# Kernel optimization log

Measured on AMD Instinct MI355X. Metric: run time of the kernel, lower is better.

The kernel has to match this reference:

```python
import jax, jax.numpy as jnp
import numpy as np

LOWERSIZE = 40


def setup_inputs() -> dict:
    key = jax.random.key(0)
    ks = jax.random.split(key, 6)
    N, x_dim, y_dim = 2048, 768, 768
    return {
        "x_samples": jax.random.normal(ks[0], (N, x_dim), dtype=jnp.float32),
        "y_samples": jax.random.normal(ks[1], (N, y_dim), dtype=jnp.float32),
        "W1": jax.random.normal(ks[2], (LOWERSIZE, x_dim + y_dim), dtype=jnp.float32) * 0.02,
        "b1": jax.random.normal(ks[3], (LOWERSIZE,), dtype=jnp.float32) * 0.02,
        "W2": jax.random.normal(ks[4], (1, LOWERSIZE), dtype=jnp.float32) * 0.02,
        "b2": jax.random.normal(ks[5], (1,), dtype=jnp.float32) * 0.02,
    }


def reference(x_samples, y_samples, W1, b1, W2, b2):
    # F(z) = W2 @ relu(W1 @ z + b1) + b2, z = cat(x, y)
    N = y_samples.shape[0]
    x_dim = x_samples.shape[1]
    W1x = W1[:, :x_dim]   # [40, x_dim]
    W1y = W1[:, x_dim:]   # [40, y_dim]

    # Diagonal term T0: F(cat(x_i, y_i)) -> [N, 1]
    h0 = jax.nn.relu(x_samples @ W1x.T + y_samples @ W1y.T + b1)
    T0 = h0 @ W2.T + b2

    # Pairwise term: T1[i, j] = F(cat(x_j, y_i)) - 1.
    # Split the first Linear over x and y to avoid materializing the
    # [N, N, x_dim+y_dim] concatenation (same math, linearity of W1).
    hx = x_samples @ W1x.T  # [N, 40]
    hy = y_samples @ W1y.T  # [N, 40]
    h = jax.nn.relu(hy[:, None, :] + hx[None, :, :] + b1)  # [N, N, 40]
    T1 = (h @ W2.T + b2 - 1.0)[..., 0]  # [N, N]

    lse = jax.nn.logsumexp(T1, axis=1) - jnp.log(jnp.float32(N))  # [N]
    lower_bound = T0.mean() - jnp.exp(lse).mean()
    return lower_bound
```

## Files before the change

kernel.cpp:

```cpp
#include <hip/hip_runtime.h>

#define NROWS 2048
#define KDIM  768
#define L     40
#define HN    (NROWS * L)

#define OPB   10
#define RPB   32
#define WF4   192

__global__ __launch_bounds__(256) void k_proj(const float* __restrict__ x,
                                              const float* __restrict__ y,
                                              const float* __restrict__ W1,
                                              const float* __restrict__ b1,
                                              float* __restrict__ hxb,
                                              float* __restrict__ hy) {
    const int og    = blockIdx.y;
    const int which = blockIdx.z;
    const float* __restrict__ A = which ? y : x;
    const int tid = threadIdx.x;
    const int r   = tid & 31;
    const int s   = tid >> 5;
    const int row0 = blockIdx.x * RPB;
    const int o0   = og * OPB;

    __shared__ float4 wlds[OPB * WF4];

    const float4* W1f4 = (const float4*)W1;
    for (int i = tid; i < OPB * WF4; i += 256) {
        int ol = i / WF4, q = i - ol * WF4;
        wlds[ol * WF4 + q] = W1f4[(size_t)(o0 + ol) * 384 + which * WF4 + q];
    }

    const float4* arow = (const float4*)(A + (size_t)(row0 + r) * KDIM) + s * 24;

    float acc[OPB];
#pragma unroll
    for (int ol = 0; ol < OPB; ++ol) acc[ol] = 0.f;

    float4 aA[8], aB[8];
#pragma unroll
    for (int j = 0; j < 8; ++j) aA[j] = arow[j];
    __syncthreads();

#define COMPUTE(AR, C) do {                                                  \
    _Pragma("unroll") for (int ol = 0; ol < OPB; ++ol) {                     \
        const float4* wp = &wlds[ol * WF4 + s * 24 + (C) * 8];               \
        float sacc = 0.f;                                                    \
        _Pragma("unroll") for (int j = 0; j < 8; ++j) {                      \
            float4 w = wp[j];                                                \
            sacc += AR[j].x * w.x + AR[j].y * w.y                            \
                  + AR[j].z * w.z + AR[j].w * w.w;                           \
        }                                                                    \
        acc[ol] += sacc;                                                     \
    } } while (0)

#pragma unroll
    for (int j = 0; j < 8; ++j) aB[j] = arow[8 + j];
    COMPUTE(aA, 0);
#pragma unroll
    for (int j = 0; j < 8; ++j) aA[j] = arow[16 + j];
    COMPUTE(aB, 1);
    COMPUTE(aA, 2);
#undef COMPUTE

    __syncthreads();
    float* red = (float*)wlds;
#pragma unroll
    for (int ol = 0; ol < OPB; ++ol)
        red[(ol * 8 + s) * 32 + r] = acc[ol];
    __syncthreads();

    for (int idx = tid; idx < RPB * OPB; idx += 256) {
        int rr = idx / OPB, ol = idx - rr * OPB;
        float v = 0.f;
#pragma unroll
        for (int ss = 0; ss < 8; ++ss)
            v += red[(ol * 8 + ss) * 32 + rr];
        int o = o0 + ol;
        if (!which) {
            hxb[(size_t)(row0 + rr) * L + o] = v + b1[o];
        } else {
            hy[(size_t)(row0 + rr) * L + o] = v;
        }
    }
}

#define BI 128
#define BJ 64
#define STRD 44

__global__ __launch_bounds__(512, 4) void k_pair(const float* __restrict__ hxb,
                                                 const float* __restrict__ hy,
                                                 const float* __restrict__ W2,
                                                 const float* __restrict__ b2p,
                                                 float* __restrict__ pairE,
                                                 float* __restrict__ pairT) {
    __shared__ float shy[BI * STRD];
    __shared__ float shx[BJ * STRD];
    __shared__ float sw2[STRD];
    __shared__ float red[16];

    const int tid = threadIdx.x;
    const int i0 = blockIdx.x * BI;
    const int j0 = blockIdx.y * BJ;

    for (int idx = tid; idx < BI * 10; idx += 512) {
        int rr = idx / 10, c = idx - rr * 10;
        float4 v = ((const float4*)(hy + (size_t)i0 * L))[idx];
        *(float4*)(shy + rr * STRD + c * 4) = v;
    }
    for (int idx = tid; idx < BJ * 10; idx += 512) {
        int rr = idx / 10, c = idx - rr * 10;
        float4 v = ((const float4*)(hxb + (size_t)j0 * L))[idx];
        *(float4*)(shx + rr * STRD + c * 4) = v;
    }
    if (tid < 10) ((float4*)sw2)[tid] = ((const float4*)W2)[tid];
    __syncthreads();

    const int tx = tid & 15, ty = tid >> 4;

    float acc[4][4];
#pragma unroll
    for (int u = 0; u < 4; ++u)
#pragma unroll
        for (int v = 0; v < 4; ++v) acc[u][v] = 0.f;

    float4 ayA[4], axA[4], wA4;
    float4 ayB[4], axB[4], wB4;

#define LOADF(AY, AX, W4, K4) do {                                          \
    W4 = *(const float4*)(sw2 + (K4) * 4);                                  \
    _Pragma("unroll") for (int u_ = 0; u_ < 4; ++u_)                        \
        AY[u_] = *(const float4*)(shy + (ty + 32 * u_) * STRD + (K4) * 4);  \
    _Pragma("unroll") for (int v_ = 0; v_ < 4; ++v_)                        \
        AX[v_] = *(const float4*)(shx + (tx + 16 * v_) * STRD + (K4) * 4);  \
} while (0)

#define FMAF(AY, AX, W4) do {                                               \
    _Pragma("unroll") for (int u_ = 0; u_ < 4; ++u_)                        \
    _Pragma("unroll") for (int v_ = 0; v_ < 4; ++v_) {                      \
        float t;                                                            \
        t = AY[u_].x + AX[v_].x; t = fmaxf(t, 0.f); acc[u_][v_] += t * W4.x;\
        t = AY[u_].y + AX[v_].y; t = fmaxf(t, 0.f); acc[u_][v_] += t * W4.y;\
        t = AY[u_].z + AX[v_].z; t = fmaxf(t, 0.f); acc[u_][v_] += t * W4.z;\
        t = AY[u_].w + AX[v_].w; t = fmaxf(t, 0.f); acc[u_][v_] += t * W4.w;\
    }                                                                       \
} while (0)

    LOADF(ayA, axA, wA4, 0);
    LOADF(ayB, axB, wB4, 1);
    FMAF(ayA, axA, wA4); LOADF(ayA, axA, wA4, 2);
    FMAF(ayB, axB, wB4); LOADF(ayB, axB, wB4, 3);
    FMAF(ayA, axA, wA4); LOADF(ayA, axA, wA4, 4);
    FMAF(ayB, axB, wB4); LOADF(ayB, axB, wB4, 5);
    FMAF(ayA, axA, wA4); LOADF(ayA, axA, wA4, 6);
    FMAF(ayB, axB, wB4); LOADF(ayB, axB, wB4, 7);
    FMAF(ayA, axA, wA4); LOADF(ayA, axA, wA4, 8);
    FMAF(ayB, axB, wB4); LOADF(ayB, axB, wB4, 9);
    FMAF(ayA, axA, wA4);
    FMAF(ayB, axB, wB4);

#undef LOADF
#undef FMAF

    const float b2v = b2p[0];
    const float c1  = b2v - 1.f;
    float sumE = 0.f, sumT = 0.f;
#pragma unroll
    for (int u = 0; u < 4; ++u)
#pragma unroll
        for (int v = 0; v < 4; ++v) {
            int gi = i0 + ty + 32 * u;
            int gj = j0 + tx + 16 * v;
            float val = acc[u][v];
            if (gi == gj) sumT += val + b2v;
            sumE += __expf(val + c1);
        }

#pragma unroll
    for (int off = 32; off > 0; off >>= 1) {
        sumE += __shfl_down(sumE, off);
        sumT += __shfl_down(sumT, off);
    }
    int wid = tid >> 6;
    if ((tid & 63) == 0) { red[wid] = sumE; red[8 + wid] = sumT; }
    __syncthreads();
    if (tid == 0) {
        float e = 0.f, t = 0.f;
#pragma unroll
        for (int q = 0; q < 8; ++q) { e += red[q]; t += red[8 + q]; }
        int bid = blockIdx.y * gridDim.x + blockIdx.x;
        pairE[bid] = e;
        pairT[bid] = t;
    }
}

__global__ __launch_bounds__(512) void k_fin(const float* __restrict__ pairE,
                                             const float* __restrict__ pairT,
                                             float* __restrict__ out) {
    __shared__ float red[16];
    const int tid = threadIdx.x;
    float e = pairE[tid];
    float t = pairT[tid];
#pragma unroll
    for (int off = 32; off > 0; off >>= 1) {
        e += __shfl_down(e, off);
        t += __shfl_down(t, off);
    }
    int wid = tid >> 6;
    if ((tid & 63) == 0) { red[wid] = e; red[8 + wid] = t; }
    __syncthreads();
    if (tid == 0) {
        float se = 0.f, st = 0.f;
#pragma unroll
        for (int q = 0; q < 8; ++q) { se += red[q]; st += red[8 + q]; }
        const float invN = 1.0f / (float)NROWS;
        out[0] = st * invN - se * invN * invN;
    }
}

extern "C" void kernel_launch(void* const* d_in, const int* in_sizes, int n_in,
                              void* d_out, int out_size, void* d_ws, size_t ws_size,
                              hipStream_t stream) {
    const float* x  = (const float*)d_in[0];
    const float* y  = (const float*)d_in[1];
    const float* W1 = (const float*)d_in[2];
    const float* b1 = (const float*)d_in[3];
    const float* W2 = (const float*)d_in[4];
    const float* b2 = (const float*)d_in[5];
    float* out = (float*)d_out;

    float* wsf   = (float*)d_ws;
    float* hxb   = wsf;
    float* hy    = hxb + HN;
    float* pairE = hy + HN;
    float* pairT = pairE + 512;

    k_proj<<<dim3(NROWS / RPB, 4, 2), 256, 0, stream>>>(x, y, W1, b1, hxb, hy);
    k_pair<<<dim3(NROWS / BI, NROWS / BJ), 512, 0, stream>>>(hxb, hy, W2, b2, pairE, pairT);
    k_fin<<<1, 512, 0, stream>>>(pairE, pairT, out);
}
```

Measured before the change: 95.85 us.

## Restructure projection kernel to 16-row tiles with 16 K-segments and padded LDS

```diff
diff --git a/kernel.cpp b/kernel.cpp
--- a/kernel.cpp
+++ b/kernel.cpp
@@ -6,77 +6,69 @@
 #define HN    (NROWS * L)
 
 #define OPB   10
-#define RPB   32
-#define WF4   192
-
-__global__ __launch_bounds__(256) void k_proj(const float* __restrict__ x,
-                                              const float* __restrict__ y,
-                                              const float* __restrict__ W1,
-                                              const float* __restrict__ b1,
-                                              float* __restrict__ hxb,
-                                              float* __restrict__ hy) {
+#define RPB   16
+#define SEGS  16
+#define SF4   12
+#define SP4   13
+
+__global__ __launch_bounds__(256, 4) void k_proj(const float* __restrict__ x,
+                                                 const float* __restrict__ y,
+                                                 const float* __restrict__ W1,
+                                                 const float* __restrict__ b1,
+                                                 float* __restrict__ hxb,
+                                                 float* __restrict__ hy) {
     const int og    = blockIdx.y;
     const int which = blockIdx.z;
     const float* __restrict__ A = which ? y : x;
     const int tid = threadIdx.x;
-    const int r   = tid & 31;
-    const int s   = tid >> 5;
+    const int s   = tid & 15;
+    const int r   = tid >> 4;
     const int row0 = blockIdx.x * RPB;
     const int o0   = og * OPB;
 
-    __shared__ float4 wlds[OPB * WF4];
+    __shared__ float4 wlds[OPB * SEGS * SP4];
+
+    const float4* arow = (const float4*)(A + (size_t)(row0 + r) * KDIM) + s * SF4;
+    float4 a[SF4];
+#pragma unroll
+    for (int j = 0; j < SF4; ++j) a[j] = arow[j];
 
     const float4* W1f4 = (const float4*)W1;
-    for (int i = tid; i < OPB * WF4; i += 256) {
-        int ol = i / WF4, q = i - ol * WF4;
-        wlds[ol * WF4 + q] = W1f4[(size_t)(o0 + ol) * 384 + which * WF4 + q];
-    }
-
-    const float4* arow = (const float4*)(A + (size_t)(row0 + r) * KDIM) + s * 24;
+    for (int i = tid; i < OPB * 192; i += 256) {
+        int ol = i / 192, q = i - ol * 192;
+        int ss = q / SF4, j = q - ss * SF4;
+        wlds[(ol * SEGS + ss) * SP4 + j] =
+            W1f4[(size_t)(o0 + ol) * 384 + which * 192 + q];
+    }
+    __syncthreads();
 
     float acc[OPB];
 #pragma unroll
-    for (int ol = 0; ol < OPB; ++ol) acc[ol] = 0.f;
-
-    float4 aA[8], aB[8];
-#pragma unroll
-    for (int j = 0; j < 8; ++j) aA[j] = arow[j];
-    __syncthreads();
-
-#define COMPUTE(AR, C) do {                                                  \
-    _Pragma("unroll") for (int ol = 0; ol < OPB; ++ol) {                     \
-        const float4* wp = &wlds[ol * WF4 + s * 24 + (C) * 8];               \
-        float sacc = 0.f;                                                    \
-        _Pragma("unroll") for (int j = 0; j < 8; ++j) {                      \
-            float4 w = wp[j];                                                \
-            sacc += AR[j].x * w.x + AR[j].y * w.y                            \
-                  + AR[j].z * w.z + AR[j].w * w.w;                           \
-        }                                                                    \
-        acc[ol] += sacc;                                                     \
-    } } while (0)
-
-#pragma unroll
-    for (int j = 0; j < 8; ++j) aB[j] = arow[8 + j];
-    COMPUTE(aA, 0);
-#pragma unroll
-    for (int j = 0; j < 8; ++j) aA[j] = arow[16 + j];
-    COMPUTE(aB, 1);
-    COMPUTE(aA, 2);
-#undef COMPUTE
+    for (int ol = 0; ol < OPB; ++ol) {
+        const float4* wp = &wlds[(ol * SEGS + s) * SP4];
+        float sacc = 0.f;
+#pragma unroll
+        for (int j = 0; j < SF4; ++j) {
+            float4 w = wp[j];
+            sacc += a[j].x * w.x + a[j].y * w.y
+                  + a[j].z * w.z + a[j].w * w.w;
+        }
+        acc[ol] = sacc;
+    }
 
     __syncthreads();
     float* red = (float*)wlds;
 #pragma unroll
     for (int ol = 0; ol < OPB; ++ol)
-        red[(ol * 8 + s) * 32 + r] = acc[ol];
-    __syncthreads();
-
-    for (int idx = tid; idx < RPB * OPB; idx += 256) {
-        int rr = idx / OPB, ol = idx - rr * OPB;
+        red[(ol * SEGS + s) * 17 + r] = acc[ol];
+    __syncthreads();
+
+    if (tid < RPB * OPB) {
+        int rr = tid / OPB, ol = tid - rr * OPB;
         float v = 0.f;
 #pragma unroll
-        for (int ss = 0; ss < 8; ++ss)
-            v += red[(ol * 8 + ss) * 32 + rr];
+        for (int ss = 0; ss < SEGS; ++ss)
+            v += red[(ol * SEGS + ss) * 17 + rr];
         int o = o0 + ol;
         if (!which) {
             hxb[(size_t)(row0 + rr) * L + o] = v + b1[o];
```

After: 93.69 us. -2.3%, faster.
